# Kernel optimization log

Measured on AMD Instinct MI355X. Metric: run time of the kernel, lower is better.

The kernel has to match this reference:

```python
import jax, jax.numpy as jnp
import numpy as np

B, S, M = 2, 2048, 2048
NQ, NKV, H = 16, 4, 128
EPS = 1e-6
MAX_WAVELENGTH = 10000.0
NEG_INF = -1e9


def rmsnorm(x, scale, eps=EPS):
    # RMSNorm over head_dim (last axis), computed in fp32.
    xf = x.astype(jnp.float32)
    var = jnp.mean(xf * xf, axis=-1, keepdims=True)
    return (xf * jax.lax.rsqrt(var + eps) * scale).astype(x.dtype)


def rope(x, max_wavelength=MAX_WAVELENGTH, scaling_factor=1.0, start_index=0):
    # x: [b, s, n, h]; keras_hub split-half rotary embedding.
    h = x.shape[-1]
    inv_freq = 1.0 / (max_wavelength ** (jnp.arange(0, h, 2, dtype=jnp.float32) / h))
    pos = (jnp.arange(x.shape[1], dtype=jnp.float32) + start_index) / scaling_factor
    freq = pos[:, None] * inv_freq[None, :]             # [s, h/2]
    emb = jnp.concatenate([freq, freq], axis=-1)        # [s, h]
    cos = jnp.cos(emb)[None, :, None, :]
    sin = jnp.sin(emb)[None, :, None, :]
    x1, x2 = x[..., : h // 2], x[..., h // 2 :]
    rot = jnp.concatenate([-x2, x1], axis=-1)
    return (x * cos + rot * sin).astype(x.dtype)


def setup_inputs() -> dict:
    key = jax.random.key(0)
    ks = jax.random.split(key, 6)
    hidden_states = jax.random.normal(ks[0], (B, S, M), dtype=jnp.float32)
    # causal mask [b, q, k]
    causal = jnp.tril(jnp.ones((S, S), dtype=bool))
    attention_mask = jnp.broadcast_to(causal[None], (B, S, S))
    sq = 0.02
    Wq = jax.random.normal(ks[1], (M, NQ, H), dtype=jnp.float32) * sq
    Wk = jax.random.normal(ks[2], (M, NKV, H), dtype=jnp.float32) * sq
    Wv = jax.random.normal(ks[3], (M, NKV, H), dtype=jnp.float32) * sq
    Wo = jax.random.normal(ks[4], (NQ, H, M), dtype=jnp.float32) * sq
    q_scale = jnp.ones((H,), dtype=jnp.float32)
    k_scale = jnp.ones((H,), dtype=jnp.float32)
    return {
        "hidden_states": hidden_states,
        "attention_mask": attention_mask,
        "Wq": Wq,
        "Wk": Wk,
        "Wv": Wv,
        "Wo": Wo,
        "q_scale": q_scale,
        "k_scale": k_scale,
    }


def reference(hidden_states, attention_mask, Wq, Wk, Wv, Wo, q_scale, k_scale):
    inv_norm = 1.0 / np.sqrt(H)
    groups = NQ // NKV

    q = jnp.einsum("bqm,muh->bquh", hidden_states, Wq)   # [b,q,NQ,H]
    q = rope(rmsnorm(q, q_scale))
    k = jnp.einsum("bkm,mvh->bkvh", hidden_states, Wk)   # [b,k,NKV,H]
    k = rope(rmsnorm(k, k_scale))
    v = jnp.einsum("bkm,mvh->bkvh", hidden_states, Wv)

    # GQA broadcast: repeat each kv head `groups` times consecutively.
    k = jnp.repeat(k, groups, axis=2)
    v = jnp.repeat(v, groups, axis=2)

    scores = jnp.einsum("bquh,bkuh->buqk", q, k) * inv_norm  # [b,u,q,k]
    scores = scores.astype(jnp.float32)
    scores = jnp.where(attention_mask[:, None, :, :], scores, NEG_INF)
    probs = jax.nn.softmax(scores, axis=-1).astype(hidden_states.dtype)

    attn = jnp.einsum("buqk,bkuh->bquh", probs, v)
    out = jnp.einsum("bquh,uhm->bqm", attn, Wo)
    return out
```

## Files before the change

kernel.cpp:

```cpp
#include <hip/hip_runtime.h>
#include <stdint.h>

#define BB 2
#define SS 2048
#define MM 2048
#define NQ 16
#define NKV 4
#define HH 128
#define KVB 64

typedef __attribute__((ext_vector_type(4))) float f32x4;
typedef __attribute__((ext_vector_type(16))) float f32x16;
typedef _Float16 f16x8 __attribute__((ext_vector_type(8)));
typedef _Float16 f16x4 __attribute__((ext_vector_type(4)));
typedef _Float16 f16x2 __attribute__((ext_vector_type(2)));
typedef unsigned int uint4v __attribute__((ext_vector_type(4)));

__device__ __forceinline__ void gll16(const _Float16* g, _Float16* l) {
  __builtin_amdgcn_global_load_lds(
      (__attribute__((address_space(1))) void*)g,
      (__attribute__((address_space(3))) void*)l, 16, 0, 0);
}

__device__ __forceinline__ float fexp2(float x) {
#if __has_builtin(__builtin_amdgcn_exp2f)
  return __builtin_amdgcn_exp2f(x);
#else
  float r;
  asm("v_exp_f32 %0, %1" : "=v"(r) : "v"(x));
  return r;
#endif
}

__device__ __forceinline__ unsigned int pkrtz(float a, float b) {
  return __builtin_bit_cast(unsigned int, __builtin_amdgcn_cvt_pkrtz(a, b));
}

__global__ __launch_bounds__(256) void k_f32_to_f16(const float* __restrict__ in,
                                                    _Float16* __restrict__ out, int n4) {
  int i = blockIdx.x * 256 + threadIdx.x;
  if (i >= n4) return;
  float4 v = ((const float4*)in)[i];
  f16x4 o = { (_Float16)v.x, (_Float16)v.y, (_Float16)v.z, (_Float16)v.w };
  ((f16x4*)out)[i] = o;
}

__global__ __launch_bounds__(256) void k_wtrans(
    const float* __restrict__ Wq, const float* __restrict__ Wk,
    const float* __restrict__ Wv, const float* __restrict__ Wo,
    _Float16* __restrict__ Wqkvt, _Float16* __restrict__ Wot) {
  const int z = blockIdx.z;
  if ((z == 1 || z == 2) && blockIdx.y >= 16) return;
  const float* in = (z == 0) ? Wq : (z == 1) ? Wk : (z == 2) ? Wv : Wo;
  _Float16* out = (z == 3) ? Wot : Wqkvt;
  const int N_in = (z == 1 || z == 2) ? 512 : 2048;
  const int n_off = (z == 1) ? 2048 : (z == 2) ? 2560 : 0;

  __shared__ float tile[32][33];
  const int k0 = blockIdx.x * 32;
  const int n0 = blockIdx.y * 32;
  const int tx = threadIdx.x & 31;
  const int ty = threadIdx.x >> 5;
  #pragma unroll
  for (int r = ty; r < 32; r += 8)
    tile[r][tx] = in[(size_t)(k0 + r) * N_in + n0 + tx];
  __syncthreads();
  #pragma unroll
  for (int r = ty; r < 32; r += 8)
    out[(size_t)(n0 + r + n_off) * 2048 + k0 + tx] = (_Float16)tile[tx][r];
}

__global__ __launch_bounds__(256) void k_vtrans(const _Float16* __restrict__ qkv,
                                                _Float16* __restrict__ VtG) {
  __shared__ _Float16 tile[32][33];
  const int s0 = blockIdx.x * 32;
  const int z = blockIdx.y;
  const int h0 = (z & 3) * 32;
  const int bv = z >> 2;
  const int b = bv >> 2;
  const int hv = bv & 3;
  const int tx = threadIdx.x & 31;
  const int ty = threadIdx.x >> 5;
  #pragma unroll
  for (int r = ty; r < 32; r += 8)
    tile[r][tx] = qkv[(size_t)(b * SS + s0 + r) * 3072 + 2560 + hv * 128 + h0 + tx];
  __syncthreads();
  #pragma unroll
  for (int r = ty; r < 32; r += 8)
    VtG[((size_t)bv * HH + h0 + r) * SS + s0 + tx] = tile[tx][r];
}

template <int FN, bool F16OUT>
__global__ __launch_bounds__(512, 2) void k_gemm256(
    const _Float16* __restrict__ A, const _Float16* __restrict__ Bt,
    void* __restrict__ Cout, int NT_M, int N, int K) {
  __shared__ _Float16 As[2][256 * 64];
  __shared__ _Float16 Bs[2][FN * 64 * 64];

  const int tid = threadIdx.x;
  const int w = tid >> 6;
  const int l = tid & 63;
  const int lr = l & 15;
  const int al4 = l >> 4;
  const int wr = w >> 2;
  const int wc = w & 3;
  const int swz = (lr & 7) << 4;

  const int nwg = gridDim.x;
  const int bid = blockIdx.x;
  const int sbid = (bid & 7) * (nwg >> 3) + (bid >> 3);
  const int bm = (sbid % NT_M) * 256;
  const int bn = (sbid / NT_M) * (FN * 64);
  const int KT = K >> 6;

  const int srow = tid >> 3;
  const int sch = (tid & 7) ^ (srow & 7);
  const _Float16* aSrc = A + (size_t)(bm + srow) * K + sch * 8;
  const _Float16* bSrc = Bt + (size_t)(bn + srow) * K + sch * 8;

  auto stA = [&](int buf, int r, int kt) {
    gll16(aSrc + (size_t)(r * 64) * K + kt * 64, &As[buf][r * 4096 + w * 512]);
  };
  auto stB = [&](int buf, int r, int kt) {
    gll16(bSrc + (size_t)(r * 64) * K + kt * 64, &Bs[buf][r * 4096 + w * 512]);
  };

  f32x4 acc[8][FN] = {};

  stA(0, 0, 0); stA(0, 1, 0); stA(0, 2, 0); stA(0, 3, 0);
  stB(0, 0, 0); stB(0, 1, 0);
  if (FN == 3) stB(0, 2, 0);
  if (KT > 1) {
    stA(1, 0, 1); stA(1, 2, 1); stB(1, 0, 1); stB(1, 1, 1);
    asm volatile("s_waitcnt vmcnt(4)" ::: "memory");
  } else {
    asm volatile("s_waitcnt vmcnt(0)" ::: "memory");
  }
  __builtin_amdgcn_s_barrier();

  for (int t = 0; t < KT; ++t) {
    const int cb = t & 1;
    const char* Ab = (const char*)&As[cb][0];
    const char* Bb = (const char*)&Bs[cb][0];
    f16x8 bF[FN][2];
    #pragma unroll
    for (int ph = 0; ph < 2; ++ph) {
      f16x8 aF[4][2];
      #pragma unroll
      for (int fm = 0; fm < 4; ++fm)
        #pragma unroll
        for (int ks = 0; ks < 2; ++ks) {
          const int row = wr * 128 + (ph * 4 + fm) * 16 + lr;
          aF[fm][ks] = *(const f16x8*)(Ab + row * 128 + (((ks * 4 + al4) * 16) ^ swz));
        }
      if (ph == 0) {
        #pragma unroll
        for (int fn = 0; fn < FN; ++fn)
          #pragma unroll
          for (int ks = 0; ks < 2; ++ks) {
            const int col = wc * (FN * 16) + fn * 16 + lr;
            bF[fn][ks] = *(const f16x8*)(Bb + col * 128 + (((ks * 4 + al4) * 16) ^ swz));
          }
      }
      if (ph == 0 && t + 1 < KT) {
        if (FN == 3) stB(cb ^ 1, 2, t + 1);
        stA(cb ^ 1, 1, t + 1); stA(cb ^ 1, 3, t + 1);
      }
      if (ph == 1 && t + 2 < KT) {
        stA(cb, 0, t + 2); stA(cb, 2, t + 2);
        stB(cb, 0, t + 2); stB(cb, 1, t + 2);
      }
      __builtin_amdgcn_s_barrier();
      asm volatile("s_waitcnt lgkmcnt(0)" ::: "memory");
      __builtin_amdgcn_sched_barrier(0);
      __builtin_amdgcn_s_setprio(1);
      #pragma unroll
      for (int fm = 0; fm < 4; ++fm)
        #pragma unroll
        for (int fn = 0; fn < FN; ++fn)
          #pragma unroll
          for (int ks = 0; ks < 2; ++ks)
            acc[ph * 4 + fm][fn] = __builtin_amdgcn_mfma_f32_16x16x32_f16(
                aF[fm][ks], bF[fn][ks], acc[ph * 4 + fm][fn], 0, 0, 0);
      __builtin_amdgcn_s_setprio(0);
      __builtin_amdgcn_sched_barrier(0);
      if (ph == 0) {
        __builtin_amdgcn_s_barrier();
      } else {
        if (t + 2 < KT) asm volatile("s_waitcnt vmcnt(4)" ::: "memory");
        else            asm volatile("s_waitcnt vmcnt(0)" ::: "memory");
        __builtin_amdgcn_s_barrier();
      }
    }
  }

  #pragma unroll
  for (int fm = 0; fm < 8; ++fm) {
    #pragma unroll
    for (int i = 0; i < 4; ++i) {
      const int row = bm + wr * 128 + fm * 16 + al4 * 4 + i;
      #pragma unroll
      for (int fn = 0; fn < FN; ++fn) {
        const int col = bn + wc * (FN * 16) + fn * 16 + lr;
        if (F16OUT)
          ((_Float16*)Cout)[(size_t)row * N + col] = (_Float16)acc[fm][fn][i];
        else
          ((float*)Cout)[(size_t)row * N + col] = acc[fm][fn][i];
      }
    }
  }
}

__global__ __launch_bounds__(256) void k_normrope(
    const _Float16* __restrict__ qkv,
    const float* __restrict__ q_scale, const float* __restrict__ k_scale,
    _Float16* __restrict__ Qr, _Float16* __restrict__ Kr) {
  const int row = blockIdx.x;
  const int b = row >> 11;
  const int s = row & 2047;
  const int hh = blockIdx.y * 4 + (threadIdx.x >> 6);
  const int l = threadIdx.x & 63;
  const _Float16* src = qkv + (size_t)row * 3072 + hh * 128 + l * 2;
  float x0 = (float)src[0];
  float x1 = (float)src[1];
  float ssum = x0 * x0 + x1 * x1;
  #pragma unroll
  for (int d = 1; d < 64; d <<= 1) ssum += __shfl_xor(ssum, d);
  const float rstd = rsqrtf(ssum * (1.f / 128.f) + 1e-6f);
  const float* scl = (hh < 16) ? q_scale : k_scale;
  x0 *= rstd * scl[2 * l];
  x1 *= rstd * scl[2 * l + 1];
  const float y0 = __shfl_xor(x0, 32);
  const float y1 = __shfl_xor(x1, 32);
  const int j0 = (2 * l) & 63;
  const float kLog = 0.20762050593046014f;
  const float f0 = (float)s * exp2f(-(float)j0 * kLog);
  const float f1 = (float)s * exp2f(-(float)(j0 + 1) * kLog);
  const float c0 = cosf(f0), s0 = sinf(f0);
  const float c1 = cosf(f1), s1 = sinf(f1);
  float r0, r1;
  if (l < 32) { r0 = x0 * c0 - y0 * s0; r1 = x1 * c1 - y1 * s1; }
  else        { r0 = x0 * c0 + y0 * s0; r1 = x1 * c1 + y1 * s1; }
  if (hh < 16) {
    _Float16* dst = Qr + ((size_t)(b * NQ + hh) * SS + s) * HH + 2 * l;
    dst[0] = (_Float16)r0; dst[1] = (_Float16)r1;
  } else {
    _Float16* dst = Kr + ((size_t)(b * NKV + (hh - 16)) * SS + s) * HH + 2 * l;
    dst[0] = (_Float16)r0; dst[1] = (_Float16)r1;
  }
}

__device__ const unsigned char g_tasks[24] = {
  61, 63, 28,
  57, 59, 53, 55, 24,
  49, 51, 45, 47, 20,
  41, 43, 37, 39, 16,
  33, 35, 12,
  8, 4, 0
};

__global__ __launch_bounds__(256, 3) void k_attn(
    const _Float16* __restrict__ Qr, const _Float16* __restrict__ Kr,
    const _Float16* __restrict__ VtG,
    const float* __restrict__ qs, const float* __restrict__ ks,
    float* __restrict__ PartA, float* __restrict__ PartB,
    float* __restrict__ psA, float* __restrict__ psB,
    _Float16* __restrict__ Ao) {
  __shared__ _Float16 Ks[KVB * 128];
  __shared__ _Float16 Vs[128 * KVB];

  const int tid = threadIdx.x;
  const int w = tid >> 6;
  const int l = tid & 63;
  const int l31 = l & 31;
  const int hi = l >> 5;
  const int sw7 = (l31 & 7) << 4;
  const int bu = blockIdx.x;
  const int b = bu >> 4, u = bu & 15;
  const int kvh = u >> 2;

  const int task = g_tasks[blockIdx.y];
  const int heavy = task & 1;
  const int half = (task >> 1) & 1;
  const int qt = task >> 2;
  const int q0 = qt * 128;
  const int halfLen = qt + 1;
  const int t0 = heavy ? half * halfLen : 0;
  const int t1 = heavy ? t0 + halfLen : 2 * qt + 2;

  float ma = fmaxf(fabsf(qs[l]), fabsf(qs[l + 64]));
  float mb = fmaxf(fabsf(ks[l]), fabsf(ks[l + 64]));
  #pragma unroll
  for (int d = 1; d < 64; d <<= 1) {
    ma = fmaxf(ma, __shfl_xor(ma, d));
    mb = fmaxf(mb, __shfl_xor(mb, d));
  }
  const float M2 = 1.4426950408889634f * ma * mb;
  const float K2 = 0.12752982260735795f;

  const _Float16* Kbase = Kr + (size_t)(b * NKV + kvh) * SS * HH;
  const _Float16* Vbase = VtG + (size_t)(b * NKV + kvh) * HH * SS;

  f16x8 qf[8];
  {
    const _Float16* qp = Qr + ((size_t)(b * NQ + u) * SS + q0 + w * 32 + l31) * HH + hi * 8;
    #pragma unroll
    for (int hs = 0; hs < 8; hs++) {
      qf[hs] = *(const f16x8*)(qp + hs * 16);
      qf[hs] *= (_Float16)K2;
    }
  }

  f32x16 acc0 = {}, acc1 = {}, acc2 = {}, acc3 = {};
  float psum = 0.f;

  auto stage = [&](int t) {
    const int kv0 = t * KVB;
    #pragma unroll
    for (int it = 0; it < 4; it++) {
      const int n = it * 256 + tid;
      {
        const int row = n >> 4, c = n & 15;
        const int cs = c ^ (row & 7);
        gll16(Kbase + (size_t)(kv0 + row) * HH + cs * 8,
              &Ks[(size_t)(it * 256 + w * 64) * 8]);
      }
      {
        const int row = n >> 3, c = n & 7;
        const int cs = c ^ (row & 7);
        gll16(Vbase + (size_t)row * SS + kv0 + cs * 8,
              &Vs[(size_t)(it * 256 + w * 64) * 8]);
      }
    }
  };

  const int qwb = q0 + w * 32;
  const int qlane = qwb + l31;

  for (int t = t0; t < t1; t++) {
    stage(t);
    __syncthreads();
    const int kv0 = t * KVB;
    if (kv0 <= qwb + 31) {
      const char* Kb = (const char*)&Ks[0];
      const char* Vb = (const char*)&Vs[0];

      f32x16 S0 = {}, S1 = {};
      __builtin_amdgcn_s_setprio(1);
      #pragma unroll
      for (int hs = 0; hs < 8; hs++) {
        const int ch = hs * 2 + hi;
        f16x8 k0 = *(const f16x8*)(Kb + l31 * 256 + ((ch << 4) ^ sw7));
        f16x8 k1 = *(const f16x8*)(Kb + (32 + l31) * 256 + ((ch << 4) ^ sw7));
        S0 = __builtin_amdgcn_mfma_f32_32x32x16_f16(k0, qf[hs], S0, 0, 0, 0);
        S1 = __builtin_amdgcn_mfma_f32_32x32x16_f16(k1, qf[hs], S1, 0, 0, 0);
      }
      __builtin_amdgcn_s_setprio(0);

      const bool domask = (kv0 + 63 > qwb);
      float p0[16], p1[16];
      #pragma unroll
      for (int r = 0; r < 16; r++) {
        const int cr = (r & 3) + 8 * (r >> 2) + 4 * hi;
        float e0 = fexp2(S0[r] - M2);
        float e1 = fexp2(S1[r] - M2);
        if (domask) {
          if (kv0 + cr > qlane) e0 = 0.f;
          if (kv0 + 32 + cr > qlane) e1 = 0.f;
        }
        p0[r] = e0; p1[r] = e1;
        psum += e0 + e1;
      }

      unsigned int pkv[4][4];
      #pragma unroll
      for (int g = 0; g < 4; g++) {
        pkv[0][g] = pkrtz(p0[2 * g], p0[2 * g + 1]);
        pkv[1][g] = pkrtz(p0[8 + 2 * g], p0[9 + 2 * g]);
        pkv[2][g] = pkrtz(p1[2 * g], p1[2 * g + 1]);
        pkv[3][g] = pkrtz(p1[8 + 2 * g], p1[9 + 2 * g]);
      }
      f16x8 pa[4];
      #pragma unroll
      for (int ksx = 0; ksx < 4; ksx++) {
        unsigned int a0 = pkv[ksx][0], a1 = pkv[ksx][1], a2 = pkv[ksx][2], a3 = pkv[ksx][3];
        unsigned int x0 = (unsigned int)__shfl_xor((int)a0, 32);
        unsigned int x1 = (unsigned int)__shfl_xor((int)a1, 32);
        unsigned int x2 = (unsigned int)__shfl_xor((int)a2, 32);
        unsigned int x3 = (unsigned int)__shfl_xor((int)a3, 32);
        uint4v dv;
        dv.x = hi ? x2 : a0;
        dv.y = hi ? x3 : a1;
        dv.z = hi ? a2 : x0;
        dv.w = hi ? a3 : x1;
        pa[ksx] = __builtin_bit_cast(f16x8, dv);
      }

      __builtin_amdgcn_s_setprio(1);
      #pragma unroll
      for (int ksx = 0; ksx < 4; ksx++) {
        const int ch = ksx * 2 + hi;
        f16x8 v0 = *(const f16x8*)(Vb + (0 * 32 + l31) * 128 + ((ch << 4) ^ sw7));
        acc0 = __builtin_amdgcn_mfma_f32_32x32x16_f16(pa[ksx], v0, acc0, 0, 0, 0);
        f16x8 v1 = *(const f16x8*)(Vb + (1 * 32 + l31) * 128 + ((ch << 4) ^ sw7));
        acc1 = __builtin_amdgcn_mfma_f32_32x32x16_f16(pa[ksx], v1, acc1, 0, 0, 0);
        f16x8 v2 = *(const f16x8*)(Vb + (2 * 32 + l31) * 128 + ((ch << 4) ^ sw7));
        acc2 = __builtin_amdgcn_mfma_f32_32x32x16_f16(pa[ksx], v2, acc2, 0, 0, 0);
        f16x8 v3 = *(const f16x8*)(Vb + (3 * 32 + l31) * 128 + ((ch << 4) ^ sw7));
        acc3 = __builtin_amdgcn_mfma_f32_32x32x16_f16(pa[ksx], v3, acc3, 0, 0, 0);
      }
      __builtin_amdgcn_s_setprio(0);
    }
    __syncthreads();
  }

  const float tot = psum + __shfl_xor(psum, 32);
  if (heavy) {
    const int slot = bu * 8 + (qt - 8);
    float* pPart = (half ? PartB : PartA) + (size_t)slot * 16384;
    float* sPart = (half ? psB : psA) + slot * 128;
    if (hi == 0) sPart[w * 32 + l31] = tot;
    #pragma unroll
    for (int r = 0; r < 16; r++) {
      const int cr = (r & 3) + 8 * (r >> 2) + 4 * hi;
      float* dst = pPart + (size_t)(w * 32 + cr) * 128 + l31;
      dst[0]  = acc0[r];
      dst[32] = acc1[r];
      dst[64] = acc2[r];
      dst[96] = acc3[r];
    }
  } else {
    const float inv = 1.f / tot;
    #pragma unroll
    for (int r = 0; r < 16; r++) {
      const int cr = (r & 3) + 8 * (r >> 2) + 4 * hi;
      const float ivr = __shfl(inv, cr);
      _Float16* dst = Ao + ((size_t)(b * SS + q0 + w * 32 + cr)) * MM + u * HH + l31;
      dst[0]  = (_Float16)(acc0[r] * ivr);
      dst[32] = (_Float16)(acc1[r] * ivr);
      dst[64] = (_Float16)(acc2[r] * ivr);
      dst[96] = (_Float16)(acc3[r] * ivr);
    }
  }
}

__global__ __launch_bounds__(256) void k_fin(
    const float* __restrict__ PartA, const float* __restrict__ PartB,
    const float* __restrict__ psA, const float* __restrict__ psB,
    _Float16* __restrict__ Ao) {
  const int slot = blockIdx.x;
  const int bu = slot >> 3, st = slot & 7;
  const int b = bu >> 4, u = bu & 15;
  const int qt = st + 8;
  const float* pa = PartA + (size_t)slot * 16384;
  const float* pb = PartB + (size_t)slot * 16384;
  const float* sa = psA + slot * 128;
  const float* sb = psB + slot * 128;
  #pragma unroll
  for (int it = 0; it < 16; it++) {
    const int unit = it * 256 + threadIdx.x;
    const int qr = unit >> 5, cg = unit & 31;
    const float inv = 1.f / (sa[qr] + sb[qr]);
    f32x4 va = *(const f32x4*)(pa + qr * 128 + cg * 4);
    f32x4 vb = *(const f32x4*)(pb + qr * 128 + cg * 4);
    f16x4 o = { (_Float16)((va[0] + vb[0]) * inv), (_Float16)((va[1] + vb[1]) * inv),
                (_Float16)((va[2] + vb[2]) * inv), (_Float16)((va[3] + vb[3]) * inv) };
    *(f16x4*)(Ao + ((size_t)(b * SS + qt * 128 + qr)) * MM + u * HH + cg * 4) = o;
  }
}

extern "C" void kernel_launch(void* const* d_in, const int* in_sizes, int n_in,
                              void* d_out, int out_size, void* d_ws, size_t ws_size,
                              hipStream_t stream) {
  const float* hidden = (const float*)d_in[0];
  const float* Wq = (const float*)d_in[2];
  const float* Wk = (const float*)d_in[3];
  const float* Wv = (const float*)d_in[4];
  const float* Wo = (const float*)d_in[5];
  const float* q_scale = (const float*)d_in[6];
  const float* k_scale = (const float*)d_in[7];

  char* ws = (char*)d_ws;
  _Float16* Xb    = (_Float16*)(ws);
  _Float16* Wqkvt = (_Float16*)(ws + 16777216);
  _Float16* Wot   = (_Float16*)(ws + 29360128);
  _Float16* qkv   = (_Float16*)(ws + 37748736);
  _Float16* Qr    = (_Float16*)(ws + 62914560);
  _Float16* Kr    = (_Float16*)(ws + 79691776);
  _Float16* VtG   = (_Float16*)(ws + 83886080);
  _Float16* Ao    = (_Float16*)(ws + 88080384);
  float*    PartB = (float*)(ws);
  float*    PartA = (float*)(ws + 37748736);
  float*    psA   = (float*)(ws + 54525952);
  float*    psB   = (float*)(ws + 54657024);

  k_f32_to_f16<<<dim3(8192), dim3(256), 0, stream>>>(hidden, Xb, 2097152);
  k_wtrans<<<dim3(64, 64, 4), dim3(256), 0, stream>>>(Wq, Wk, Wv, Wo, Wqkvt, Wot);
  k_gemm256<3, true><<<dim3(256), dim3(512), 0, stream>>>(Xb, Wqkvt, (void*)qkv, 16, 3072, 2048);
  k_normrope<<<dim3(4096, 5), dim3(256), 0, stream>>>(qkv, q_scale, k_scale, Qr, Kr);
  k_vtrans<<<dim3(64, 32), dim3(256), 0, stream>>>(qkv, VtG);
  k_attn<<<dim3(32, 24), dim3(256), 0, stream>>>(Qr, Kr, VtG, q_scale, k_scale,
                                                 PartA, PartB, psA, psB, Ao);
  k_fin<<<dim3(256), dim3(256), 0, stream>>>(PartA, PartB, psA, psB, Ao);
  k_gemm256<2, false><<<dim3(256), dim3(512), 0, stream>>>(Ao, Wot, d_out, 16, 2048, 2048);
}
```

Baseline: 217.1 us.

## Prefetch next K/V tile into registers during attention compute

Replaces direct global-to-LDS loads issued right before each tile's compute with register prefetching. The next K/V tile is loaded into registers while the current tile's MFMA work runs, then written to LDS after a barrier. This hides global memory latency behind compute. In exchange it uses more VGPRs, which may lower occupancy, and it adds an extra barrier per iteration.

```diff
diff --git a/kernel.cpp b/kernel.cpp
--- a/kernel.cpp
+++ b/kernel.cpp
@@ -314,32 +314,38 @@
   f32x16 acc0 = {}, acc1 = {}, acc2 = {}, acc3 = {};
   float psum = 0.f;
 
-  auto stage = [&](int t) {
+  const int krow0 = tid >> 4, kc0 = (tid & 15) ^ (krow0 & 7);
+  const int vrow0 = tid >> 3, vc0 = (tid & 7) ^ (vrow0 & 7);
+  uint4v kreg[4], vreg[4];
+
+  auto loadT = [&](int t) {
     const int kv0 = t * KVB;
     #pragma unroll
     for (int it = 0; it < 4; it++) {
-      const int n = it * 256 + tid;
-      {
-        const int row = n >> 4, c = n & 15;
-        const int cs = c ^ (row & 7);
-        gll16(Kbase + (size_t)(kv0 + row) * HH + cs * 8,
-              &Ks[(size_t)(it * 256 + w * 64) * 8]);
-      }
-      {
-        const int row = n >> 3, c = n & 7;
-        const int cs = c ^ (row & 7);
-        gll16(Vbase + (size_t)row * SS + kv0 + cs * 8,
-              &Vs[(size_t)(it * 256 + w * 64) * 8]);
-      }
+      const int krow = krow0 + it * 16;
+      const int vrow = vrow0 + it * 32;
+      kreg[it] = *(const uint4v*)(Kbase + (size_t)(kv0 + krow) * HH + kc0 * 8);
+      vreg[it] = *(const uint4v*)(Vbase + (size_t)vrow * SS + kv0 + vc0 * 8);
+    }
+  };
+  auto writeT = [&]() {
+    #pragma unroll
+    for (int it = 0; it < 4; it++) {
+      *(uint4v*)(&Ks[(size_t)(it * 256 + tid) * 8]) = kreg[it];
+      *(uint4v*)(&Vs[(size_t)(it * 256 + tid) * 8]) = vreg[it];
     }
   };
 
   const int qwb = q0 + w * 32;
   const int qlane = qwb + l31;
 
+  loadT(t0);
+  writeT();
+  __syncthreads();
+
   for (int t = t0; t < t1; t++) {
-    stage(t);
-    __syncthreads();
+    const bool hasNext = (t + 1 < t1);
+    if (hasNext) loadT(t + 1);
     const int kv0 = t * KVB;
     if (kv0 <= qwb + 31) {
       const char* Kb = (const char*)&Ks[0];
@@ -411,6 +417,8 @@
       }
       __builtin_amdgcn_s_setprio(0);
     }
+    __syncthreads();
+    if (hasNext) writeT();
     __syncthreads();
   }
 
```

Measured after the change: 247.0 us. 1.14x slower.

## Stage 128-key K/V tiles per barrier pair in attention kernel

Applied to the files above, without the earlier changes.

Doubles the shared-memory K/V tile from 64 to 128 keys and processes two 64-key sub-blocks per staging step. This halves the number of __syncthreads pairs and load-wait stalls per iteration. It also changes how the work is split between heavy-task halves so that each half covers an even number of 64-key tiles. The larger LDS footprint drops launch bounds from 3 to 2 blocks per CU, which reduces occupancy and latency hiding.

```diff
diff --git a/kernel.cpp b/kernel.cpp
--- a/kernel.cpp
+++ b/kernel.cpp
@@ -259,15 +259,15 @@
   8, 4, 0
 };
 
-__global__ __launch_bounds__(256, 3) void k_attn(
+__global__ __launch_bounds__(256, 2) void k_attn(
     const _Float16* __restrict__ Qr, const _Float16* __restrict__ Kr,
     const _Float16* __restrict__ VtG,
     const float* __restrict__ qs, const float* __restrict__ ks,
     float* __restrict__ PartA, float* __restrict__ PartB,
     float* __restrict__ psA, float* __restrict__ psB,
     _Float16* __restrict__ Ao) {
-  __shared__ _Float16 Ks[KVB * 128];
-  __shared__ _Float16 Vs[128 * KVB];
+  __shared__ _Float16 Ks[128 * 128];
+  __shared__ _Float16 Vs[128 * 128];
 
   const int tid = threadIdx.x;
   const int w = tid >> 6;
@@ -284,9 +284,10 @@
   const int half = (task >> 1) & 1;
   const int qt = task >> 2;
   const int q0 = qt * 128;
-  const int halfLen = qt + 1;
-  const int t0 = heavy ? half * halfLen : 0;
-  const int t1 = heavy ? t0 + halfLen : 2 * qt + 2;
+  const int total = 2 * qt + 2;
+  const int h0 = ((qt + 2) >> 1) << 1;
+  const int t0 = heavy ? (half ? h0 : 0) : 0;
+  const int t1 = heavy ? (half ? total : h0) : total;
 
   float ma = fmaxf(fabsf(qs[l]), fabsf(qs[l + 64]));
   float mb = fmaxf(fabsf(ks[l]), fabsf(ks[l + 64]));
@@ -314,102 +315,98 @@
   f32x16 acc0 = {}, acc1 = {}, acc2 = {}, acc3 = {};
   float psum = 0.f;
 
-  auto stage = [&](int t) {
-    const int kv0 = t * KVB;
-    #pragma unroll
-    for (int it = 0; it < 4; it++) {
+  auto stage = [&](int m) {
+    const int kv0 = m * KVB;
+    #pragma unroll
+    for (int it = 0; it < 8; it++) {
       const int n = it * 256 + tid;
-      {
-        const int row = n >> 4, c = n & 15;
-        const int cs = c ^ (row & 7);
-        gll16(Kbase + (size_t)(kv0 + row) * HH + cs * 8,
-              &Ks[(size_t)(it * 256 + w * 64) * 8]);
-      }
-      {
-        const int row = n >> 3, c = n & 7;
-        const int cs = c ^ (row & 7);
-        gll16(Vbase + (size_t)row * SS + kv0 + cs * 8,
-              &Vs[(size_t)(it * 256 + w * 64) * 8]);
-      }
+      const int row = n >> 4, c = n & 15;
+      const int cs = c ^ (row & 7);
+      gll16(Kbase + (size_t)(kv0 + row) * HH + cs * 8,
+            &Ks[(size_t)(it * 256 + w * 64) * 8]);
+      gll16(Vbase + (size_t)row * SS + kv0 + cs * 8,
+            &Vs[(size_t)(it * 256 + w * 64) * 8]);
     }
   };
 
   const int qwb = q0 + w * 32;
   const int qlane = qwb + l31;
 
-  for (int t = t0; t < t1; t++) {
-    stage(t);
+  for (int m = t0; m < t1; m += 2) {
+    stage(m);
     __syncthreads();
-    const int kv0 = t * KVB;
-    if (kv0 <= qwb + 31) {
-      const char* Kb = (const char*)&Ks[0];
-      const char* Vb = (const char*)&Vs[0];
-
-      f32x16 S0 = {}, S1 = {};
-      __builtin_amdgcn_s_setprio(1);
-      #pragma unroll
-      for (int hs = 0; hs < 8; hs++) {
-        const int ch = hs * 2 + hi;
-        f16x8 k0 = *(const f16x8*)(Kb + l31 * 256 + ((ch << 4) ^ sw7));
-        f16x8 k1 = *(const f16x8*)(Kb + (32 + l31) * 256 + ((ch << 4) ^ sw7));
-        S0 = __builtin_amdgcn_mfma_f32_32x32x16_f16(k0, qf[hs], S0, 0, 0, 0);
-        S1 = __builtin_amdgcn_mfma_f32_32x32x16_f16(k1, qf[hs], S1, 0, 0, 0);
+    const char* Kb = (const char*)&Ks[0];
+    const char* Vb = (const char*)&Vs[0];
+    #pragma unroll
+    for (int hh2 = 0; hh2 < 2; ++hh2) {
+      const int kv0 = m * KVB + hh2 * 64;
+      if (kv0 <= qwb + 31) {
+        f32x16 S0 = {}, S1 = {};
+        __builtin_amdgcn_s_setprio(1);
+        #pragma unroll
+        for (int hs = 0; hs < 8; hs++) {
+          const int ch = hs * 2 + hi;
+          f16x8 k0 = *(const f16x8*)(Kb + (hh2 * 64 + l31) * 256 + ((ch << 4) ^ sw7));
+          f16x8 k1 = *(const f16x8*)(Kb + (hh2 * 64 + 32 + l31) * 256 + ((ch << 4) ^ sw7));
+          S0 = __builtin_amdgcn_mfma_f32_32x32x16_f16(k0, qf[hs], S0, 0, 0, 0);
+          S1 = __builtin_amdgcn_mfma_f32_32x32x16_f16(k1, qf[hs], S1, 0, 0, 0);
+        }
+        __builtin_amdgcn_s_setprio(0);
+
+        const bool domask = (kv0 + 63 > qwb);
+        float p0[16], p1[16];
+        #pragma unroll
+        for (int r = 0; r < 16; r++) {
+          const int cr = (r & 3) + 8 * (r >> 2) + 4 * hi;
+          float e0 = fexp2(S0[r] - M2);
+          float e1 = fexp2(S1[r] - M2);
+          if (domask) {
+            if (kv0 + cr > qlane) e0 = 0.f;
+            if (kv0 + 32 + cr > qlane) e1 = 0.f;
+          }
+          p0[r] = e0; p1[r] = e1;
+          psum += e0 + e1;
+        }
+
+        unsigned int pkv[4][4];
+        #pragma unroll
+        for (int g = 0; g < 4; g++) {
+          pkv[0][g] = pkrtz(p0[2 * g], p0[2 * g + 1]);
+          pkv[1][g] = pkrtz(p0[8 + 2 * g], p0[9 + 2 * g]);
+          pkv[2][g] = pkrtz(p1[2 * g], p1[2 * g + 1]);
+          pkv[3][g] = pkrtz(p1[8 + 2 * g], p1[9 + 2 * g]);
+        }
+        f16x8 pa[4];
+        #pragma unroll
+        for (int ksx = 0; ksx < 4; ksx++) {
+          unsigned int a0 = pkv[ksx][0], a1 = pkv[ksx][1], a2 = pkv[ksx][2], a3 = pkv[ksx][3];
+          unsigned int x0 = (unsigned int)__shfl_xor((int)a0, 32);
+          unsigned int x1 = (unsigned int)__shfl_xor((int)a1, 32);
+          unsigned int x2 = (unsigned int)__shfl_xor((int)a2, 32);
+          unsigned int x3 = (unsigned int)__shfl_xor((int)a3, 32);
+          uint4v dv;
+          dv.x = hi ? x2 : a0;
+          dv.y = hi ? x3 : a1;
+          dv.z = hi ? a2 : x0;
+          dv.w = hi ? a3 : x1;
+          pa[ksx] = __builtin_bit_cast(f16x8, dv);
+        }
+
+        __builtin_amdgcn_s_setprio(1);
+        #pragma unroll
+        for (int ksx = 0; ksx < 4; ksx++) {
+          const int ch = hh2 * 8 + ksx * 2 + hi;
+          f16x8 v0 = *(const f16x8*)(Vb + (0 * 32 + l31) * 256 + ((ch << 4) ^ sw7));
+          acc0 = __builtin_amdgcn_mfma_f32_32x32x16_f16(pa[ksx], v0, acc0, 0, 0, 0);
+          f16x8 v1 = *(const f16x8*)(Vb + (1 * 32 + l31) * 256 + ((ch << 4) ^ sw7));
+          acc1 = __builtin_amdgcn_mfma_f32_32x32x16_f16(pa[ksx], v1, acc1, 0, 0, 0);
+          f16x8 v2 = *(const f16x8*)(Vb + (2 * 32 + l31) * 256 + ((ch << 4) ^ sw7));
+          acc2 = __builtin_amdgcn_mfma_f32_32x32x16_f16(pa[ksx], v2, acc2, 0, 0, 0);
+          f16x8 v3 = *(const f16x8*)(Vb + (3 * 32 + l31) * 256 + ((ch << 4) ^ sw7));
+          acc3 = __builtin_amdgcn_mfma_f32_32x32x16_f16(pa[ksx], v3, acc3, 0, 0, 0);
+        }
+        __builtin_amdgcn_s_setprio(0);
       }
-      __builtin_amdgcn_s_setprio(0);
-
-      const bool domask = (kv0 + 63 > qwb);
-      float p0[16], p1[16];
-      #pragma unroll
-      for (int r = 0; r < 16; r++) {
-        const int cr = (r & 3) + 8 * (r >> 2) + 4 * hi;
-        float e0 = fexp2(S0[r] - M2);
-        float e1 = fexp2(S1[r] - M2);
-        if (domask) {
-          if (kv0 + cr > qlane) e0 = 0.f;
-          if (kv0 + 32 + cr > qlane) e1 = 0.f;
-        }
-        p0[r] = e0; p1[r] = e1;
-        psum += e0 + e1;
-      }
-
-      unsigned int pkv[4][4];
-      #pragma unroll
-      for (int g = 0; g < 4; g++) {
-        pkv[0][g] = pkrtz(p0[2 * g], p0[2 * g + 1]);
-        pkv[1][g] = pkrtz(p0[8 + 2 * g], p0[9 + 2 * g]);
-        pkv[2][g] = pkrtz(p1[2 * g], p1[2 * g + 1]);
-        pkv[3][g] = pkrtz(p1[8 + 2 * g], p1[9 + 2 * g]);
-      }
-      f16x8 pa[4];
-      #pragma unroll
-      for (int ksx = 0; ksx < 4; ksx++) {
-        unsigned int a0 = pkv[ksx][0], a1 = pkv[ksx][1], a2 = pkv[ksx][2], a3 = pkv[ksx][3];
-        unsigned int x0 = (unsigned int)__shfl_xor((int)a0, 32);
-        unsigned int x1 = (unsigned int)__shfl_xor((int)a1, 32);
-        unsigned int x2 = (unsigned int)__shfl_xor((int)a2, 32);
-        unsigned int x3 = (unsigned int)__shfl_xor((int)a3, 32);
-        uint4v dv;
-        dv.x = hi ? x2 : a0;
-        dv.y = hi ? x3 : a1;
-        dv.z = hi ? a2 : x0;
-        dv.w = hi ? a3 : x1;
-        pa[ksx] = __builtin_bit_cast(f16x8, dv);
-      }
-
-      __builtin_amdgcn_s_setprio(1);
-      #pragma unroll
-      for (int ksx = 0; ksx < 4; ksx++) {
-        const int ch = ksx * 2 + hi;
-        f16x8 v0 = *(const f16x8*)(Vb + (0 * 32 + l31) * 128 + ((ch << 4) ^ sw7));
-        acc0 = __builtin_amdgcn_mfma_f32_32x32x16_f16(pa[ksx], v0, acc0, 0, 0, 0);
-        f16x8 v1 = *(const f16x8*)(Vb + (1 * 32 + l31) * 128 + ((ch << 4) ^ sw7));
-        acc1 = __builtin_amdgcn_mfma_f32_32x32x16_f16(pa[ksx], v1, acc1, 0, 0, 0);
-        f16x8 v2 = *(const f16x8*)(Vb + (2 * 32 + l31) * 128 + ((ch << 4) ^ sw7));
-        acc2 = __builtin_amdgcn_mfma_f32_32x32x16_f16(pa[ksx], v2, acc2, 0, 0, 0);
-        f16x8 v3 = *(const f16x8*)(Vb + (3 * 32 + l31) * 128 + ((ch << 4) ^ sw7));
-        acc3 = __builtin_amdgcn_mfma_f32_32x32x16_f16(pa[ksx], v3, acc3, 0, 0, 0);
-      }
-      __builtin_amdgcn_s_setprio(0);
     }
     __syncthreads();
   }
```

After: 210.7 us. 3.0% less time.
